# Performance work log

Measured on AMD Instinct MI355X. Metric: run time of the kernel, lower is better.

## Reference

```python
import jax, jax.numpy as jnp
import numpy as np

NEG_SLOPE = 0.2


def gat_conv(x, src, dst, W, att_src, att_dst, bias, heads, out_ch, concat):
    """PyG-style GATConv (eval mode, self-loops already appended to src/dst)."""
    N = x.shape[0]
    h = (x @ W).reshape(N, heads, out_ch)                      # [N,H,C]
    a_src = jnp.einsum('nhc,hc->nh', h, att_src)               # [N,H]
    a_dst = jnp.einsum('nhc,hc->nh', h, att_dst)               # [N,H]
    e = jax.nn.leaky_relu(a_src[src] + a_dst[dst], NEG_SLOPE)  # [E,H]
    # numerically-stable softmax segmented by destination node
    emax = jax.ops.segment_max(e, dst, num_segments=N)         # [N,H]
    e = jnp.exp(e - emax[dst])
    denom = jax.ops.segment_sum(e, dst, num_segments=N)
    alpha = e / (denom[dst] + 1e-16)                           # [E,H]
    msg = h[src] * alpha[..., None]                            # [E,H,C]
    out = jax.ops.segment_sum(msg, dst, num_segments=N)        # [N,H,C]
    out = out.reshape(N, heads * out_ch) if concat else out.mean(axis=1)
    return out + bias


def setup_inputs() -> dict:
    key = jax.random.key(0)
    ks = jax.random.split(key, 9)
    N, E, IN, OUT = 100000, 1600000, 128, 40
    H1, C1 = 8, 8
    x = jax.random.normal(ks[0], (N, IN), dtype=jnp.float32)
    edge_index = jax.random.randint(ks[1], (2, E), 0, N, dtype=jnp.int64)
    s = 0.1
    return {
        'x': x,
        'edge_index': edge_index,
        'W1': jax.random.normal(ks[2], (IN, H1 * C1), dtype=jnp.float32) * s,
        'att_src1': jax.random.normal(ks[3], (H1, C1), dtype=jnp.float32) * s,
        'att_dst1': jax.random.normal(ks[4], (H1, C1), dtype=jnp.float32) * s,
        'b1': jnp.zeros((H1 * C1,), dtype=jnp.float32),
        'W2': jax.random.normal(ks[5], (H1 * C1, OUT), dtype=jnp.float32) * s,
        'att_src2': jax.random.normal(ks[6], (1, OUT), dtype=jnp.float32) * s,
        'att_dst2': jax.random.normal(ks[7], (1, OUT), dtype=jnp.float32) * s,
        'b2': jnp.zeros((OUT,), dtype=jnp.float32),
    }


def reference(x, edge_index, W1, att_src1, att_dst1, b1, W2, att_src2, att_dst2, b2):
    N = x.shape[0]
    loops = jnp.arange(N, dtype=edge_index.dtype)
    src = jnp.concatenate([edge_index[0], loops])  # self-loops (PyG default)
    dst = jnp.concatenate([edge_index[1], loops])
    h = gat_conv(x, src, dst, W1, att_src1, att_dst1, b1, 8, 8, True)
    h = jax.nn.elu(h)  # dropout is identity in eval mode
    out = gat_conv(h, src, dst, W2, att_src2, att_dst2, b2, 1, W2.shape[1], False)
    return jax.nn.log_softmax(out, axis=-1)
```

## Files before the change

### kernel.cpp

```cpp
#include <hip/hip_runtime.h>
#include <math.h>

#define NEG_SLOPE 0.2f
#define BSHIFT 8
#define MAXBUK 512

typedef __attribute__((ext_vector_type(8))) short short8;
typedef __attribute__((ext_vector_type(4))) float floatx4;

static __device__ __forceinline__ float lrelu_exp(float e) {
    e = fmaxf(e, NEG_SLOPE * e);
    return __expf(e);
}

static __device__ __forceinline__ short f2bf(float f) {
    union { float f; unsigned u; } v; v.f = f;
    unsigned r = v.u + 0x7FFFu + ((v.u >> 16) & 1u);
    return (short)(r >> 16);
}
static __device__ __forceinline__ float bf2f(unsigned short s) {
    union { float f; unsigned u; } v;
    v.u = ((unsigned)s) << 16;
    return v.f;
}
static __device__ __forceinline__ float bfpair_lo(unsigned v) {
    union { float f; unsigned u; } x; x.u = v << 16; return x.f;
}
static __device__ __forceinline__ float bfpair_hi(unsigned v) {
    union { float f; unsigned u; } x; x.u = v & 0xffff0000u; return x.f;
}
static __device__ __forceinline__ void splitbf(float f, short& hi, short& lo) {
    hi = f2bf(f);
    lo = f2bf(f - bf2f((unsigned short)hi));
}


__global__ __launch_bounds__(512) void k_hist(const int* __restrict__ dst, int E, int CHUNK,
                                              int NBLK, int NBUK, int* __restrict__ blockhist) {
    __shared__ int hist[MAXBUK];
    int t = threadIdx.x, b = blockIdx.x;
    for (int i = t; i < NBUK; i += 512) hist[i] = 0;
    __syncthreads();
    int e0 = b * CHUNK, e1 = e0 + CHUNK; if (e1 > E) e1 = E;
    for (int e = e0 + t; e < e1; e += 512) atomicAdd(&hist[dst[e] >> BSHIFT], 1);
    __syncthreads();
    for (int i = t; i < NBUK; i += 512) blockhist[(size_t)i * NBLK + b] = hist[i];
}

__global__ __launch_bounds__(256) void k_colscan(int* __restrict__ blockhist,
                                                 int* __restrict__ btot, int NBLK) {
    int bucket = blockIdx.x, t = threadIdx.x;
    int lane = t & 63, wv = t >> 6;
    __shared__ int wsum[4];
    __shared__ int carry_s;
    if (t == 0) carry_s = 0;
    __syncthreads();
    for (int base = 0; base < NBLK; base += 256) {
        int idx = base + t;
        int v = (idx < NBLK) ? blockhist[(size_t)bucket * NBLK + idx] : 0;
        int s = v;
#pragma unroll
        for (int o = 1; o < 64; o <<= 1) {
            int u = __shfl_up(s, o, 64);
            if (lane >= o) s += u;
        }
        if (lane == 63) wsum[wv] = s;
        __syncthreads();
        int b0 = 0;
#pragma unroll
        for (int w = 0; w < 4; ++w) b0 += (w < wv) ? wsum[w] : 0;
        int excl = s + b0 - v + carry_s;
        if (idx < NBLK) blockhist[(size_t)bucket * NBLK + idx] = excl;
        __syncthreads();
        if (t == 255) carry_s += s + b0;
        __syncthreads();
    }
    if (t == 0) btot[bucket] = carry_s;
}

__global__ __launch_bounds__(512) void k_bucket_scan(const int* __restrict__ btot,
                                                     int* __restrict__ bucketbase, int NBUK) {
    __shared__ int sh[512];
    int t = threadIdx.x;
    int v = (t < NBUK) ? btot[t] : 0;
    sh[t] = v;
    __syncthreads();
#pragma unroll
    for (int o = 1; o < 512; o <<= 1) {
        int u = (t >= o) ? sh[t - o] : 0;
        __syncthreads();
        sh[t] += u;
        __syncthreads();
    }
    if (t < NBUK) bucketbase[t] = sh[t] - v;
    if (t == NBUK - 1) bucketbase[NBUK] = sh[t];
}

__global__ __launch_bounds__(512) void k_partition(const int* __restrict__ src,
                                                   const int* __restrict__ dst, int E, int CHUNK,
                                                   int NBLK, int NBUK,
                                                   const int* __restrict__ blockhist,
                                                   const int* __restrict__ bucketbase,
                                                   unsigned* __restrict__ packed) {
    __shared__ int cur[MAXBUK];
    int t = threadIdx.x, b = blockIdx.x;
    for (int i = t; i < NBUK; i += 512)
        cur[i] = blockhist[(size_t)i * NBLK + b] + bucketbase[i];
    __syncthreads();
    int e0 = b * CHUNK, e1 = e0 + CHUNK; if (e1 > E) e1 = E;
    for (int e = e0 + t; e < e1; e += 512) {
        int d = dst[e], s = src[e];
        int pos = atomicAdd(&cur[d >> BSHIFT], 1);
        packed[pos] = ((unsigned)s << 8) | ((unsigned)d & 255u);
    }
}

__global__ __launch_bounds__(256) void k_fine(const unsigned* __restrict__ packed,
                                              const int* __restrict__ bucketbase,
                                              int* __restrict__ offsets,
                                              int* __restrict__ csr_src,
                                              int N, int NBUK) {
    __shared__ int fcnt[256];
    __shared__ int wsum[4];
    int bucket = blockIdx.x, t = threadIdx.x;
    int lo = bucket << BSHIFT;
    int nn = N - lo; if (nn > 256) nn = 256;
    int ebase = bucketbase[bucket];
    int ecnt = bucketbase[bucket + 1] - ebase;
    fcnt[t] = 0;
    __syncthreads();
    for (int i = t; i < ecnt; i += 256) {
        unsigned p = packed[ebase + i];
        atomicAdd(&fcnt[p & 255u], 1);
    }
    __syncthreads();
    int v = fcnt[t];
    int lane = t & 63, wv = t >> 6;
    int s = v;
#pragma unroll
    for (int o = 1; o < 64; o <<= 1) {
        int u = __shfl_up(s, o, 64);
        if (lane >= o) s += u;
    }
    if (lane == 63) wsum[wv] = s;
    __syncthreads();
    int base = 0;
#pragma unroll
    for (int w = 0; w < 4; ++w) base += (w < wv) ? wsum[w] : 0;
    int excl = s + base - v;
    if (t < nn) offsets[lo + t] = ebase + excl;
    if (bucket == NBUK - 1 && t == 0) offsets[N] = ebase + ecnt;
    __syncthreads();
    fcnt[t] = excl;
    __syncthreads();
    for (int i = t; i < ecnt; i += 256) {
        unsigned p = packed[ebase + i];
        int pos = atomicAdd(&fcnt[p & 255u], 1);
        csr_src[ebase + pos] = (int)(p >> 8);
    }
}

__global__ __launch_bounds__(256) void k_splitW2(const float* __restrict__ W2,
                                                 short* __restrict__ w2h,
                                                 short* __restrict__ w2l) {
    int i = blockIdx.x * 256 + threadIdx.x;
    if (i < 64 * 48) {
        int row = i / 48, col = i % 48;
        short hi = 0, lo = 0;
        if (col < 40) splitbf(W2[row * 40 + col], hi, lo);
        w2h[i] = hi; w2l[i] = lo;
    }
}

__global__ __launch_bounds__(256) void k_gemm1(const float* __restrict__ x,
                                               const float* __restrict__ W1,
                                               const float* __restrict__ att_s,
                                               const float* __restrict__ att_d,
                                               unsigned short* __restrict__ h1b,
                                               float* __restrict__ a_s1,
                                               float* __restrict__ a_d1, int N) {
    int tid = threadIdx.x, wave = tid >> 6, lane = tid & 63;
    int n16 = lane & 15, q = lane >> 4;
    int nb = blockIdx.x * 64 + wave * 16;
    if (nb >= N) return;

    short8 bfr[4][4];
#pragma unroll
    for (int ct = 0; ct < 4; ++ct) {
        int n = ct * 16 + n16;
#pragma unroll
        for (int kc = 0; kc < 4; ++kc) {
            int k0 = kc * 32 + q * 8;
            short8 b;
#pragma unroll
            for (int j = 0; j < 8; ++j) b[j] = f2bf(W1[(k0 + j) * 64 + n]);
            bfr[ct][kc] = b;
        }
    }

    int arow = nb + n16; if (arow >= N) arow = N - 1;
    const float* xr = x + (size_t)arow * 128 + q * 8;
    short8 afr[4];
#pragma unroll
    for (int kc = 0; kc < 4; ++kc) {
        float4 u0 = *(const float4*)(xr + kc * 32);
        float4 u1 = *(const float4*)(xr + kc * 32 + 4);
        short8 a;
        a[0] = f2bf(u0.x); a[1] = f2bf(u0.y); a[2] = f2bf(u0.z); a[3] = f2bf(u0.w);
        a[4] = f2bf(u1.x); a[5] = f2bf(u1.y); a[6] = f2bf(u1.z); a[7] = f2bf(u1.w);
        afr[kc] = a;
    }

    floatx4 acc[4];
#pragma unroll
    for (int ct = 0; ct < 4; ++ct) {
        floatx4 c = {0.f, 0.f, 0.f, 0.f};
#pragma unroll
        for (int kc = 0; kc < 4; ++kc)
            c = __builtin_amdgcn_mfma_f32_16x16x32_bf16(afr[kc], bfr[ct][kc], c, 0, 0, 0);
        acc[ct] = c;
    }

#pragma unroll
    for (int ct = 0; ct < 4; ++ct) {
#pragma unroll
        for (int r = 0; r < 4; ++r) {
            int row = nb + q * 4 + r;
            if (row < N) h1b[(size_t)row * 64 + ct * 16 + n16] = (unsigned short)f2bf(acc[ct][r]);
        }
    }

#pragma unroll
    for (int ct = 0; ct < 4; ++ct) {
        float as = att_s[ct * 16 + n16];
        float ad = att_d[ct * 16 + n16];
#pragma unroll
        for (int r = 0; r < 4; ++r) {
            float ps = acc[ct][r] * as;
            float pd = acc[ct][r] * ad;
#pragma unroll
            for (int m = 1; m < 8; m <<= 1) {
                ps += __shfl_xor(ps, m, 64);
                pd += __shfl_xor(pd, m, 64);
            }
            int row = nb + q * 4 + r;
            if ((n16 & 7) == 0 && row < N) {
                int h = 2 * ct + (n16 >> 3);
                a_s1[row * 8 + h] = ps;
                a_d1[row * 8 + h] = pd;
            }
        }
    }
}

__global__ __launch_bounds__(256) void k_agg1(const unsigned short* __restrict__ h1b,
                                              const float* __restrict__ a_s1,
                                              const float* __restrict__ a_d1,
                                              const int* __restrict__ offsets,
                                              const int* __restrict__ csr_src,
                                              const float* __restrict__ b1,
                                              float* __restrict__ y1, int N) {
    int wave = threadIdx.x >> 6, lane = threadIdx.x & 63;
    int d = blockIdx.x * 4 + wave;
    if (d >= N) return;
    int q2 = lane >> 5;
    int c  = lane & 31;
    int h  = c >> 2;
    float ad = a_d1[d * 8 + h];
    float accx = 0.f, accy = 0.f;
    float wsum_l = 0.f;
    if (q2 == 0) {
        float w0 = lrelu_exp(a_s1[d * 8 + h] + ad);
        unsigned v = *(const unsigned*)(h1b + (size_t)d * 64 + 2 * c);
        accx = w0 * bfpair_lo(v);
        accy = w0 * bfpair_hi(v);
        wsum_l = w0;
    }
    int i0 = offsets[d], i1 = offsets[d + 1];
    for (int base = i0; base < i1; base += 64) {
        int m = i1 - base; if (m > 64) m = 64;
        int sv = (lane < m) ? csr_src[base + lane] : 0;
        for (int j = 0; j < m; j += 16) {
            int   ei[8]; int si[8]; float ev[8]; unsigned vv[8];
#pragma unroll
            for (int u = 0; u < 8; ++u) {
                ei[u] = j + 2 * u + q2;
                si[u] = __shfl(sv, ei[u], 64);
            }
#pragma unroll
            for (int u = 0; u < 8; ++u) ev[u] = a_s1[si[u] * 8 + h] + ad;
#pragma unroll
            for (int u = 0; u < 8; ++u)
                vv[u] = *(const unsigned*)(h1b + (size_t)si[u] * 64 + 2 * c);
#pragma unroll
            for (int u = 0; u < 8; ++u) {
                float w = (ei[u] < m) ? lrelu_exp(ev[u]) : 0.f;
                wsum_l += w;
                accx = fmaf(w, bfpair_lo(vv[u]), accx);
                accy = fmaf(w, bfpair_hi(vv[u]), accy);
            }
        }
    }
    accx += __shfl_xor(accx, 32, 64);
    accy += __shfl_xor(accy, 32, 64);
    wsum_l += __shfl_xor(wsum_l, 32, 64);
    if (q2 == 0) {
        float inv = 1.f / (wsum_l + 1e-16f);
        float bx = b1[2 * c], by = b1[2 * c + 1];
        float ox = accx * inv + bx;
        float oy = accy * inv + by;
        ox = ox > 0.f ? ox : expm1f(ox);
        oy = oy > 0.f ? oy : expm1f(oy);
        float2 o2 = make_float2(ox, oy);
        *(float2*)(y1 + (size_t)d * 64 + 2 * c) = o2;
    }
}

__global__ __launch_bounds__(256) void k_gemm2(const float* __restrict__ y1,
                                               const short* __restrict__ w2h,
                                               const short* __restrict__ w2l,
                                               const float* __restrict__ att_s,
                                               const float* __restrict__ att_d,
                                               unsigned short* __restrict__ h2b,
                                               float* __restrict__ a2s,
                                               float* __restrict__ a2d, int N) {
    int tid = threadIdx.x, wave = tid >> 6, lane = tid & 63;
    int n16 = lane & 15, q = lane >> 4;
    int nb = blockIdx.x * 64 + wave * 16;
    if (nb >= N) return;

    int arow = nb + n16; if (arow >= N) arow = N - 1;
    const float* yr = y1 + (size_t)arow * 64 + q * 8;
    short8 ah[2], al[2];
#pragma unroll
    for (int kc = 0; kc < 2; ++kc) {
        float4 u0 = *(const float4*)(yr + kc * 32);
        float4 u1 = *(const float4*)(yr + kc * 32 + 4);
        short8 h, l; short hi, lo;
        splitbf(u0.x, hi, lo); h[0] = hi; l[0] = lo;
        splitbf(u0.y, hi, lo); h[1] = hi; l[1] = lo;
        splitbf(u0.z, hi, lo); h[2] = hi; l[2] = lo;
        splitbf(u0.w, hi, lo); h[3] = hi; l[3] = lo;
        splitbf(u1.x, hi, lo); h[4] = hi; l[4] = lo;
        splitbf(u1.y, hi, lo); h[5] = hi; l[5] = lo;
        splitbf(u1.z, hi, lo); h[6] = hi; l[6] = lo;
        splitbf(u1.w, hi, lo); h[7] = hi; l[7] = lo;
        ah[kc] = h; al[kc] = l;
    }

    float psr[4] = {0.f, 0.f, 0.f, 0.f}, pdr[4] = {0.f, 0.f, 0.f, 0.f};
#pragma unroll
    for (int ct = 0; ct < 3; ++ct) {
        int n = ct * 16 + n16;
        short8 bh0, bh1, bl0, bl1;
#pragma unroll
        for (int j = 0; j < 8; ++j) {
            int k0 = q * 8 + j;
            bh0[j] = w2h[k0 * 48 + n];
            bl0[j] = w2l[k0 * 48 + n];
            bh1[j] = w2h[(32 + k0) * 48 + n];
            bl1[j] = w2l[(32 + k0) * 48 + n];
        }
        floatx4 c = {0.f, 0.f, 0.f, 0.f};
        c = __builtin_amdgcn_mfma_f32_16x16x32_bf16(ah[0], bl0, c, 0, 0, 0);
        c = __builtin_amdgcn_mfma_f32_16x16x32_bf16(al[0], bh0, c, 0, 0, 0);
        c = __builtin_amdgcn_mfma_f32_16x16x32_bf16(ah[0], bh0, c, 0, 0, 0);
        c = __builtin_amdgcn_mfma_f32_16x16x32_bf16(ah[1], bl1, c, 0, 0, 0);
        c = __builtin_amdgcn_mfma_f32_16x16x32_bf16(al[1], bh1, c, 0, 0, 0);
        c = __builtin_amdgcn_mfma_f32_16x16x32_bf16(ah[1], bh1, c, 0, 0, 0);

        int col = ct * 16 + n16;
#pragma unroll
        for (int r = 0; r < 4; ++r) {
            int row = nb + q * 4 + r;
            if (col < 40 && row < N) h2b[(size_t)row * 40 + col] = (unsigned short)f2bf(c[r]);
        }
        float asv = (col < 40) ? att_s[col] : 0.f;
        float adv = (col < 40) ? att_d[col] : 0.f;
#pragma unroll
        for (int r = 0; r < 4; ++r) {
            psr[r] = fmaf(c[r], asv, psr[r]);
            pdr[r] = fmaf(c[r], adv, pdr[r]);
        }
    }
#pragma unroll
    for (int r = 0; r < 4; ++r) {
        float ps = psr[r], pd = pdr[r];
#pragma unroll
        for (int m = 1; m < 16; m <<= 1) {
            ps += __shfl_xor(ps, m, 64);
            pd += __shfl_xor(pd, m, 64);
        }
        int row = nb + q * 4 + r;
        if (n16 == 0 && row < N) { a2s[row] = ps; a2d[row] = pd; }
    }
}

__global__ __launch_bounds__(256) void k_agg2(const unsigned short* __restrict__ h2b,
                                              const float* __restrict__ a2s,
                                              const float* __restrict__ a2d,
                                              const int* __restrict__ offsets,
                                              const int* __restrict__ csr_src,
                                              const float* __restrict__ b2,
                                              float* __restrict__ out, int N) {
    int wave = threadIdx.x >> 6, lane = threadIdx.x & 63;
    int d = blockIdx.x * 4 + wave;
    if (d >= N) return;
    int t = lane / 20;
    int c = lane % 20;
    float ad = a2d[d];
    float w0 = lrelu_exp(a2s[d] + ad);
    float accx = 0.f, accy = 0.f;
    if (t == 0) {
        unsigned v = *(const unsigned*)(h2b + (size_t)d * 40 + 2 * c);
        accx = w0 * bfpair_lo(v);
        accy = w0 * bfpair_hi(v);
    }
    float wsum_l = 0.f;
    int i0 = offsets[d], i1 = offsets[d + 1];
    for (int base = i0; base < i1; base += 48) {
        int m = i1 - base; if (m > 48) m = 48;
        int sv = 0; float wv = 0.f;
        if (lane < m) {
            sv = csr_src[base + lane];
            wv = lrelu_exp(a2s[sv] + ad);
        }
        wsum_l += wv;
        for (int j = 0; j < m; j += 24) {
            int si[8]; float wq[8]; unsigned vv[8];
#pragma unroll
            for (int u = 0; u < 8; ++u) {
                int e = j + 3 * u + t;
                si[u] = __shfl(sv, e, 64);
                wq[u] = __shfl(wv, e, 64);
            }
#pragma unroll
            for (int u = 0; u < 8; ++u)
                vv[u] = *(const unsigned*)(h2b + (size_t)si[u] * 40 + 2 * c);
#pragma unroll
            for (int u = 0; u < 8; ++u) {
                accx = fmaf(wq[u], bfpair_lo(vv[u]), accx);
                accy = fmaf(wq[u], bfpair_hi(vv[u]), accy);
            }
        }
    }
    accx += __shfl(accx, lane + 20, 64) + __shfl(accx, lane + 40, 64);
    accy += __shfl(accy, lane + 20, 64) + __shfl(accy, lane + 40, 64);
#pragma unroll
    for (int mm = 1; mm < 64; mm <<= 1) wsum_l += __shfl_xor(wsum_l, mm, 64);
    float wsum = wsum_l + w0;
    bool act = (lane < 20);
    float inv = 1.f / (wsum + 1e-16f);
    float ox = act ? (accx * inv + b2[2 * c]) : -INFINITY;
    float oy = act ? (accy * inv + b2[2 * c + 1]) : -INFINITY;
    float mx = fmaxf(ox, oy);
#pragma unroll
    for (int mm = 1; mm < 64; mm <<= 1) mx = fmaxf(mx, __shfl_xor(mx, mm, 64));
    float ex = act ? (__expf(ox - mx) + __expf(oy - mx)) : 0.f;
#pragma unroll
    for (int mm = 1; mm < 64; mm <<= 1) ex += __shfl_xor(ex, mm, 64);
    if (act) {
        float lse = __logf(ex);
        float2 o2 = make_float2(ox - mx - lse, oy - mx - lse);
        *(float2*)(out + (size_t)d * 40 + 2 * c) = o2;
    }
}


extern "C" void kernel_launch(void* const* d_in, const int* in_sizes, int n_in,
                              void* d_out, int out_size, void* d_ws, size_t ws_size,
                              hipStream_t stream) {
    const float* x   = (const float*)d_in[0];
    const int*   ei  = (const int*)d_in[1];
    const float* W1  = (const float*)d_in[2];
    const float* as1 = (const float*)d_in[3];
    const float* ad1 = (const float*)d_in[4];
    const float* b1  = (const float*)d_in[5];
    const float* W2  = (const float*)d_in[6];
    const float* as2 = (const float*)d_in[7];
    const float* ad2 = (const float*)d_in[8];
    const float* b2  = (const float*)d_in[9];
    float* out = (float*)d_out;

    int N = in_sizes[0] / 128;
    int E = in_sizes[1] / 2;
    const int* src = ei;
    const int* dst = ei + E;

    int NBUK = (N + 255) >> BSHIFT;
    int CHUNK = 4096;
    int NBLK = (E + CHUNK - 1) / CHUNK;

    char* ws = (char*)d_ws;
    size_t off = 0;
    auto alloc = [&](size_t bytes) -> char* {
        char* p = ws + off;
        off += (bytes + 255) & ~(size_t)255;
        return p;
    };
    unsigned short* h1b = (unsigned short*)alloc((size_t)N * 64 * 2);
    float* a_s1    = (float*)alloc((size_t)N * 8 * 4);
    float* a_d1    = (float*)alloc((size_t)N * 8 * 4);
    float* y1      = (float*)alloc((size_t)N * 64 * 4);
    size_t shared_sz = (size_t)N * 40 * 2;
    if ((size_t)E * 4 > shared_sz) shared_sz = (size_t)E * 4;
    char*  region  = alloc(shared_sz);
    unsigned short* h2b = (unsigned short*)region;
    unsigned* packed    = (unsigned*)region;
    float* a2s     = (float*)alloc((size_t)N * 4);
    float* a2d     = (float*)alloc((size_t)N * 4);
    int*   offsets = (int*)alloc((size_t)(N + 1) * 4);
    int*   csr_src = (int*)alloc((size_t)E * 4);
    int*   blockhist  = (int*)alloc((size_t)NBUK * NBLK * 4);
    int*   btot       = (int*)alloc((size_t)NBUK * 4);
    int*   bucketbase = (int*)alloc((size_t)(NBUK + 1) * 4);
    short* w2h     = (short*)alloc((size_t)64 * 48 * 2);
    short* w2l     = (short*)alloc((size_t)64 * 48 * 2);

    int nb = (N + 3) / 4;
    int gb = (N + 63) / 64;

    k_hist<<<NBLK, 512, 0, stream>>>(dst, E, CHUNK, NBLK, NBUK, blockhist);
    k_colscan<<<NBUK, 256, 0, stream>>>(blockhist, btot, NBLK);
    k_bucket_scan<<<1, 512, 0, stream>>>(btot, bucketbase, NBUK);
    k_partition<<<NBLK, 512, 0, stream>>>(src, dst, E, CHUNK, NBLK, NBUK, blockhist,
                                          bucketbase, packed);
    k_fine<<<NBUK, 256, 0, stream>>>(packed, bucketbase, offsets, csr_src, N, NBUK);
    k_splitW2<<<12, 256, 0, stream>>>(W2, w2h, w2l);
    k_gemm1<<<gb, 256, 0, stream>>>(x, W1, as1, ad1, h1b, a_s1, a_d1, N);
    k_agg1<<<nb, 256, 0, stream>>>(h1b, a_s1, a_d1, offsets, csr_src, b1, y1, N);
    k_gemm2<<<gb, 256, 0, stream>>>(y1, w2h, w2l, as2, ad2, h2b, a2s, a2d, N);
    k_agg2<<<nb, 256, 0, stream>>>(h2b, a2s, a2d, offsets, csr_src, b2, out, N);
}
```

Before: 196.3 us.

## Remap layer-1 aggregation lanes to one head per lane with 16-byte row loads

The layer-1 aggregation kernel now gives each lane one head and 8 channels, so each lane reads 16 bytes per source row and 8 edges are processed in parallel per wave step. The old layout gave each lane 2 channels with 2 edges in flight. The change cuts redundant a_s1 loads and per-edge exp work per channel, and makes memory transactions wider. In exchange it needs a longer xor-shuffle reduction across 8 groups, more accumulator registers, and it swaps expm1f for __expf-1 in the ELU, which is slightly less accurate near zero.

```diff
diff --git a/kernel.cpp b/kernel.cpp
--- a/kernel.cpp
+++ b/kernel.cpp
@@ -263,17 +263,18 @@
     int wave = threadIdx.x >> 6, lane = threadIdx.x & 63;
     int d = blockIdx.x * 4 + wave;
     if (d >= N) return;
-    int q2 = lane >> 5;
-    int c  = lane & 31;
-    int h  = c >> 2;
+    int g = lane >> 3;
+    int h = lane & 7;
     float ad = a_d1[d * 8 + h];
-    float accx = 0.f, accy = 0.f;
+    float acc[8] = {0.f, 0.f, 0.f, 0.f, 0.f, 0.f, 0.f, 0.f};
     float wsum_l = 0.f;
-    if (q2 == 0) {
+    if (g == 0) {
         float w0 = lrelu_exp(a_s1[d * 8 + h] + ad);
-        unsigned v = *(const unsigned*)(h1b + (size_t)d * 64 + 2 * c);
-        accx = w0 * bfpair_lo(v);
-        accy = w0 * bfpair_hi(v);
+        uint4 v = *(const uint4*)(h1b + (size_t)d * 64 + 8 * h);
+        acc[0] = w0 * bfpair_lo(v.x); acc[1] = w0 * bfpair_hi(v.x);
+        acc[2] = w0 * bfpair_lo(v.y); acc[3] = w0 * bfpair_hi(v.y);
+        acc[4] = w0 * bfpair_lo(v.z); acc[5] = w0 * bfpair_hi(v.z);
+        acc[6] = w0 * bfpair_lo(v.w); acc[7] = w0 * bfpair_hi(v.w);
         wsum_l = w0;
     }
     int i0 = offsets[d], i1 = offsets[d + 1];
@@ -281,38 +282,76 @@
         int m = i1 - base; if (m > 64) m = 64;
         int sv = (lane < m) ? csr_src[base + lane] : 0;
         for (int j = 0; j < m; j += 16) {
-            int   ei[8]; int si[8]; float ev[8]; unsigned vv[8];
-#pragma unroll
-            for (int u = 0; u < 8; ++u) {
-                ei[u] = j + 2 * u + q2;
-                si[u] = __shfl(sv, ei[u], 64);
+            int eA = j + g;
+            int siA = __shfl(sv, eA, 64);
+            bool liveB = (j + 8 < m);
+            if (liveB) {
+                int eB = j + 8 + g;
+                int siB = __shfl(sv, eB, 64);
+                float evA = a_s1[siA * 8 + h] + ad;
+                float evB = a_s1[siB * 8 + h] + ad;
+                uint4 vA = *(const uint4*)(h1b + (size_t)siA * 64 + 8 * h);
+                uint4 vB = *(const uint4*)(h1b + (size_t)siB * 64 + 8 * h);
+                float wA = (eA < m) ? lrelu_exp(evA) : 0.f;
+                float wB = (eB < m) ? lrelu_exp(evB) : 0.f;
+                wsum_l += wA + wB;
+                acc[0] = fmaf(wA, bfpair_lo(vA.x), acc[0]);
+                acc[1] = fmaf(wA, bfpair_hi(vA.x), acc[1]);
+                acc[2] = fmaf(wA, bfpair_lo(vA.y), acc[2]);
+                acc[3] = fmaf(wA, bfpair_hi(vA.y), acc[3]);
+                acc[4] = fmaf(wA, bfpair_lo(vA.z), acc[4]);
+                acc[5] = fmaf(wA, bfpair_hi(vA.z), acc[5]);
+                acc[6] = fmaf(wA, bfpair_lo(vA.w), acc[6]);
+                acc[7] = fmaf(wA, bfpair_hi(vA.w), acc[7]);
+                acc[0] = fmaf(wB, bfpair_lo(vB.x), acc[0]);
+                acc[1] = fmaf(wB, bfpair_hi(vB.x), acc[1]);
+                acc[2] = fmaf(wB, bfpair_lo(vB.y), acc[2]);
+                acc[3] = fmaf(wB, bfpair_hi(vB.y), acc[3]);
+                acc[4] = fmaf(wB, bfpair_lo(vB.z), acc[4]);
+                acc[5] = fmaf(wB, bfpair_hi(vB.z), acc[5]);
+                acc[6] = fmaf(wB, bfpair_lo(vB.w), acc[6]);
+                acc[7] = fmaf(wB, bfpair_hi(vB.w), acc[7]);
+            } else {
+                float evA = a_s1[siA * 8 + h] + ad;
+                uint4 vA = *(const uint4*)(h1b + (size_t)siA * 64 + 8 * h);
+                float wA = (eA < m) ? lrelu_exp(evA) : 0.f;
+                wsum_l += wA;
+                acc[0] = fmaf(wA, bfpair_lo(vA.x), acc[0]);
+                acc[1] = fmaf(wA, bfpair_hi(vA.x), acc[1]);
+                acc[2] = fmaf(wA, bfpair_lo(vA.y), acc[2]);
+                acc[3] = fmaf(wA, bfpair_hi(vA.y), acc[3]);
+                acc[4] = fmaf(wA, bfpair_lo(vA.z), acc[4]);
+                acc[5] = fmaf(wA, bfpair_hi(vA.z), acc[5]);
+                acc[6] = fmaf(wA, bfpair_lo(vA.w), acc[6]);
+                acc[7] = fmaf(wA, bfpair_hi(vA.w), acc[7]);
             }
-#pragma unroll
-            for (int u = 0; u < 8; ++u) ev[u] = a_s1[si[u] * 8 + h] + ad;
-#pragma unroll
-            for (int u = 0; u < 8; ++u)
-                vv[u] = *(const unsigned*)(h1b + (size_t)si[u] * 64 + 2 * c);
-#pragma unroll
-            for (int u = 0; u < 8; ++u) {
-                float w = (ei[u] < m) ? lrelu_exp(ev[u]) : 0.f;
-                wsum_l += w;
-                accx = fmaf(w, bfpair_lo(vv[u]), accx);
-                accy = fmaf(w, bfpair_hi(vv[u]), accy);
-            }
-        }
-    }
-    accx += __shfl_xor(accx, 32, 64);
-    accy += __shfl_xor(accy, 32, 64);
-    wsum_l += __shfl_xor(wsum_l, 32, 64);
-    if (q2 == 0) {
+        }
+    }
+#pragma unroll
+    for (int mm = 8; mm < 64; mm <<= 1) {
+#pragma unroll
+        for (int k = 0; k < 8; ++k) acc[k] += __shfl_xor(acc[k], mm, 64);
+        wsum_l += __shfl_xor(wsum_l, mm, 64);
+    }
+    if (g == 0) {
         float inv = 1.f / (wsum_l + 1e-16f);
-        float bx = b1[2 * c], by = b1[2 * c + 1];
-        float ox = accx * inv + bx;
-        float oy = accy * inv + by;
-        ox = ox > 0.f ? ox : expm1f(ox);
-        oy = oy > 0.f ? oy : expm1f(oy);
-        float2 o2 = make_float2(ox, oy);
-        *(float2*)(y1 + (size_t)d * 64 + 2 * c) = o2;
+        float4 bA = *(const float4*)(b1 + 8 * h);
+        float4 bB = *(const float4*)(b1 + 8 * h + 4);
+        float o[8];
+        o[0] = acc[0] * inv + bA.x;
+        o[1] = acc[1] * inv + bA.y;
+        o[2] = acc[2] * inv + bA.z;
+        o[3] = acc[3] * inv + bA.w;
+        o[4] = acc[4] * inv + bB.x;
+        o[5] = acc[5] * inv + bB.y;
+        o[6] = acc[6] * inv + bB.z;
+        o[7] = acc[7] * inv + bB.w;
+#pragma unroll
+        for (int k = 0; k < 8; ++k) o[k] = o[k] > 0.f ? o[k] : (__expf(o[k]) - 1.f);
+        float4 s0 = make_float4(o[0], o[1], o[2], o[3]);
+        float4 s1 = make_float4(o[4], o[5], o[6], o[7]);
+        *(float4*)(y1 + (size_t)d * 64 + 8 * h) = s0;
+        *(float4*)(y1 + (size_t)d * 64 + 8 * h + 4) = s1;
     }
 }
 
```

Result: faster. 192.0 us (-2.2%).
